# Kernel tuning notes

Hardware: AMD Instinct MI355X
Metric: run time of the kernel (lower is better)

Reference implementation:

```python
import jax, jax.numpy as jnp
import numpy as np

B, N, D, H = 4, 2048, 768, 12
HD = D // H  # head_dim = 64


def setup_inputs() -> dict:
    key = jax.random.key(0)
    k1, k2, k3 = jax.random.split(key, 3)
    z = jax.random.normal(k1, (B, N, D), dtype=jnp.float32)
    # per-head qkv Linear weights, torch Linear convention: y = x @ W.T + b
    Wqkv = jax.random.normal(k2, (H, 3 * HD, D), dtype=jnp.float32) * 0.02
    bqkv = jnp.zeros((H, 3 * HD), dtype=jnp.float32)
    Wmsa = jax.random.normal(k3, (D, D), dtype=jnp.float32) * 0.02
    bmsa = jnp.zeros((D,), dtype=jnp.float32)
    return {"z": z, "Wqkv": Wqkv, "bqkv": bqkv, "Wmsa": Wmsa, "bmsa": bmsa}


def reference(z, Wqkv, bqkv, Wmsa, bmsa):
    # All heads' qkv projections in one einsum: [B,N,D] x [H,3hd,D] -> [B,H,N,3hd]
    qkv = jnp.einsum("bnd,hed->bhne", z, Wqkv) + bqkv[None, :, None, :]
    q, k, v = jnp.split(qkv, 3, axis=-1)  # each [B,H,N,hd]
    scale = 1.0 / jnp.sqrt(jnp.asarray(HD, dtype=z.dtype))
    scores = jnp.einsum("bhqd,bhkd->bhqk", q, k) * scale  # [B,H,N,N]
    attn = jax.nn.softmax(scores, axis=-1)
    out = jnp.einsum("bhqk,bhkd->bhqd", attn, v)  # [B,H,N,hd]
    # concat heads (head order matches the torch per-head cat)
    out = out.transpose(0, 2, 1, 3).reshape(B, N, H * HD)  # [B,N,D]
    return out @ Wmsa.T + bmsa
```

## Files before the change

### kernel.cpp

```cpp
#include <hip/hip_runtime.h>

typedef unsigned short u16;
typedef unsigned int u32;
typedef __attribute__((ext_vector_type(8))) short bf16x8;
typedef __attribute__((ext_vector_type(4))) float f32x4;

#define B_ 4
#define H_ 12
#define N_ 2048
#define D_ 768
#define HD_ 64
#define NTOK (B_ * N_)
#define NE   (H_ * 3 * HD_)

#define BK 64
#define CPITCH 144

#define QSCALE 0.18033688011112042f

__device__ __forceinline__ u16 f2bf(float f) {
    u32 u = __float_as_uint(f);
    u += 0x7fffu + ((u >> 16) & 1u);
    return (u16)(u >> 16);
}

__device__ __forceinline__ f32x4 mfma16(bf16x8 a, bf16x8 b, f32x4 c) {
    return __builtin_amdgcn_mfma_f32_16x16x32_bf16(a, b, c, 0, 0, 0);
}

__device__ __forceinline__ void g2l16(const u16* g, u16* l) {
    __builtin_amdgcn_global_load_lds(
        (const __attribute__((address_space(1))) void*)g,
        (__attribute__((address_space(3))) void*)l, 16, 0, 0);
}

#define NZ4  (NTOK * D_ / 4)
#define NWQ4 (NE * D_ / 4)
#define NWM4 (D_ * D_ / 4)
__global__ __launch_bounds__(256) void cvt_all(const float* __restrict__ z,
                                               const float* __restrict__ Wq,
                                               const float* __restrict__ Wm,
                                               u16* __restrict__ Xbf,
                                               u16* __restrict__ Wqb,
                                               u16* __restrict__ Wmb) {
    int i = blockIdx.x * blockDim.x + threadIdx.x;
    const float* src;
    u16* dst;
    int j;
    if (i < NZ4) {
        src = z; dst = Xbf; j = i;
    } else if (i < NZ4 + NWQ4) {
        src = Wq; dst = Wqb; j = i - NZ4;
    } else if (i < NZ4 + NWQ4 + NWM4) {
        src = Wm; dst = Wmb; j = i - NZ4 - NWQ4;
    } else {
        return;
    }
    float4 v = ((const float4*)src)[j];
    u32 lo = (u32)f2bf(v.x) | ((u32)f2bf(v.y) << 16);
    u32 hi = (u32)f2bf(v.z) | ((u32)f2bf(v.w) << 16);
    ((uint2*)dst)[j] = make_uint2(lo, hi);
}

#define GEMM_CORE(Xp, Wp, TM, SMELEMS)                                         \
    __shared__ u16 smem[SMELEMS];                                              \
    u16* ldsA = smem;                                          \
    u16* ldsB = smem + 2 * (TM) * BK;                         \
    const int tid = threadIdx.x;                                               \
    const int wave = tid >> 6, lane = tid & 63;                                \
    const int lrow = lane & 15, quad = lane >> 4;                              \
    const int mbase = blockIdx.x * (TM);                                       \
    const int nbase = blockIdx.y * 128;                                        \
    const int srow = tid >> 3;                                      \
    const int schunk = tid & 7;                                                \
    const int sk = (schunk ^ (srow & 7)) << 3;   \
    const int sdst = srow * BK + schunk * 8;     \
    const u16* gA = Xp + (size_t)(mbase + srow) * D_ + sk;                     \
    const u16* gB = Wp + (size_t)(nbase + srow) * D_ + sk;                     \
    const int m_ofs = (wave >> 1) * ((TM) / 2);                                \
    const int n_ofs = (wave & 1) * 64;                                         \
    const int e_ = lrow & 7;                                                   \
    const int offA0 = (m_ofs + lrow) * BK + ((quad ^ e_) << 3);                \
    const int offB0 = (n_ofs + lrow) * BK + ((quad ^ e_) << 3);                \
    f32x4 acc[(TM) / 32][4] = {};                                              \
    _Pragma("unroll") for (int i = 0; i < (TM) / 32; i++)                      \
        g2l16(gA + (size_t)(32 * i) * D_, ldsA + sdst + i * 32 * BK);          \
    _Pragma("unroll") for (int i = 0; i < 4; i++)                              \
        g2l16(gB + (size_t)(32 * i) * D_, ldsB + sdst + i * 32 * BK);          \
    for (int it = 0; it < D_ / BK; it++) {                                     \
        const int cur = it & 1;                                                \
        const int abase = cur * (TM) * BK, bbase = cur * 128 * BK;             \
        __syncthreads();   \
        if (it + 1 < D_ / BK) {                                                \
            const int kt2 = (it + 1) * BK;                                     \
            const int nb = cur ^ 1;                                            \
            _Pragma("unroll") for (int i = 0; i < (TM) / 32; i++)              \
                g2l16(gA + (size_t)(32 * i) * D_ + kt2,                        \
                      ldsA + nb * (TM) * BK + sdst + i * 32 * BK);             \
            _Pragma("unroll") for (int i = 0; i < 4; i++)                      \
                g2l16(gB + (size_t)(32 * i) * D_ + kt2,                        \
                      ldsB + nb * 128 * BK + sdst + i * 32 * BK);              \
        }                                                                      \
        _Pragma("unroll") for (int ks = 0; ks < 2; ks++) {                     \
            const int oa = abase + (offA0 ^ (ks << 5));                        \
            const int ob = bbase + (offB0 ^ (ks << 5));                        \
            bf16x8 af[(TM) / 32], bfr[4];                                      \
            _Pragma("unroll") for (int c = 0; c < (TM) / 32; c++)              \
                af[c] = *(const bf16x8*)&ldsA[oa + c * 16 * BK];               \
            _Pragma("unroll") for (int c = 0; c < 4; c++)                      \
                bfr[c] = *(const bf16x8*)&ldsB[ob + c * 16 * BK];              \
            _Pragma("unroll") for (int i = 0; i < (TM) / 32; i++)              \
                _Pragma("unroll") for (int j = 0; j < 4; j++)                  \
                    acc[i][j] = mfma16(af[i], bfr[j], acc[i][j]);              \
        }                                                                      \
    }

__global__ __launch_bounds__(256) void gemm_qkv(const u16* __restrict__ X,
                                                const u16* __restrict__ W,
                                                const float* __restrict__ bqkv,
                                                u16* __restrict__ Qs,
                                                u16* __restrict__ Ks,
                                                u16* __restrict__ Vt) {
    GEMM_CORE(X, W, 64, 24576)
    __syncthreads();
    u16* ldsC = smem;
#pragma unroll
    for (int cn = 0; cn < 4; cn++) {
        const int E = nbase + n_ofs + cn * 16;
        const int h = E / 192;
        const int rr = E - h * 192;
        const int kind = rr >> 6;
        const float bias = bqkv[E + lrow];
        if (kind == 2) {
            const int d = (rr & 63) + lrow;
#pragma unroll
            for (int cm = 0; cm < 2; cm++) {
                const int t0 = mbase + m_ofs + cm * 16 + quad * 4;
                const int b_ = t0 >> 11, n0 = t0 & (N_ - 1);
                const size_t bh = (size_t)(b_ * H_ + h);
                uint2 pk;
                pk.x = (u32)f2bf(acc[cm][cn][0] + bias) |
                       ((u32)f2bf(acc[cm][cn][1] + bias) << 16);
                pk.y = (u32)f2bf(acc[cm][cn][2] + bias) |
                       ((u32)f2bf(acc[cm][cn][3] + bias) << 16);
                *(uint2*)&Vt[(bh * HD_ + d) * N_ + n0] = pk;
            }
        } else {
            const int fcol = n_ofs + cn * 16 + lrow;
            const float scale = (kind == 0) ? QSCALE : 1.0f;
#pragma unroll
            for (int cm = 0; cm < 2; cm++)
#pragma unroll
                for (int r = 0; r < 4; r++) {
                    const int tok = m_ofs + cm * 16 + quad * 4 + r;
                    ldsC[tok * CPITCH + fcol] =
                        f2bf((acc[cm][cn][r] + bias) * scale);
                }
        }
    }
    __syncthreads();
    {
        const int tok = tid >> 2, sub = tid & 3;
        const int fh = sub >> 1, jh = sub & 1;
        const int gf = nbase + fh * 64;
        const int kind2 = (gf >> 6) % 3;
        if (kind2 != 2) {
            const int h2 = gf / 192;
            const int t = mbase + tok;
            const int b2 = t >> 11, n2 = t & (N_ - 1);
            u16* dst = (kind2 == 0 ? Qs : Ks) +
                       ((size_t)(b2 * H_ + h2) * N_ + n2) * HD_;
            const u16* src = &ldsC[tok * CPITCH + fh * 64];
#pragma unroll
            for (int j = 0; j < 4; j++)
                *(uint4*)&dst[(jh * 4 + j) * 8] =
                    *(const uint4*)&src[(jh * 4 + j) * 8];
        }
    }
}

__global__ __launch_bounds__(256) void gemm_out(const u16* __restrict__ X2,
                                                const u16* __restrict__ W,
                                                const float* __restrict__ bmsa,
                                                float* __restrict__ out) {
    GEMM_CORE(X2, W, 64, 24576)
#pragma unroll
    for (int cn = 0; cn < 4; cn++) {
        const int col = nbase + n_ofs + cn * 16 + lrow;
        const float bias = bmsa[col];
#pragma unroll
        for (int cm = 0; cm < 2; cm++) {
#pragma unroll
            for (int r = 0; r < 4; r++) {
                const int t = mbase + m_ofs + cm * 16 + quad * 4 + r;
                out[(size_t)t * D_ + col] = acc[cm][cn][r] + bias;
            }
        }
    }
}

__global__ __launch_bounds__(256, 3) void flash_attn(const u16* __restrict__ Qs,
                                                     const u16* __restrict__ Ks,
                                                     const u16* __restrict__ Vt,
                                                     u16* __restrict__ X2) {
    __shared__ u16 ldsK[2][64 * HD_];
    __shared__ u16 ldsV[2][64 * HD_];
    __shared__ u16 ldsP[4][2][16][68];
    const int tid = threadIdx.x;
    const int wave = tid >> 6, lane = tid & 63;
    const int lrow = lane & 15, quad = lane >> 4;
    const int qbase = blockIdx.x * 128 + wave * 32;
    const int bh = blockIdx.y;
    const int b = bh / H_, h = bh - b * H_;

    const u16* Kb = Ks + (size_t)bh * N_ * HD_;
    const u16* Vb = Vt + (size_t)bh * HD_ * N_;

    const int srow = tid >> 3;
    const int schunk = tid & 7;
    const int skk = (schunk ^ (srow & 7)) << 3;
    const int sdst = srow * HD_ + schunk * 8;

    bf16x8 qa[2][2];
#pragma unroll
    for (int t = 0; t < 2; t++) {
        const u16* Qb = Qs + ((size_t)bh * N_ + qbase + t * 16 + lrow) * HD_ + quad * 8;
        qa[t][0] = *(const bf16x8*)(Qb);
        qa[t][1] = *(const bf16x8*)(Qb + 32);
    }

    const int fofs = (quad ^ (lrow & 7)) << 3;
    const short onebf = (short)0x3F80;
    const bf16x8 ones = {onebf, onebf, onebf, onebf, onebf, onebf, onebf, onebf};

    f32x4 Oacc[2][4] = {};
    f32x4 lacc[2] = {};

    {
        const u16* gK = Kb + (size_t)srow * HD_ + skk;
        g2l16(gK, &ldsK[0][sdst]);
        g2l16(gK + (size_t)32 * HD_, &ldsK[0][sdst + 32 * HD_]);
        const u16* gV = Vb + (size_t)srow * N_ + skk;
        g2l16(gV, &ldsV[0][sdst]);
        g2l16(gV + (size_t)32 * N_, &ldsV[0][sdst + 32 * HD_]);
    }

    for (int it = 0; it < N_ / 64; it++) {
        const int cur = it & 1;
        __syncthreads();
        if (it + 1 < N_ / 64) {
            const int kt2 = (it + 1) << 6;
            const u16* gK = Kb + (size_t)(kt2 + srow) * HD_ + skk;
            g2l16(gK, &ldsK[cur ^ 1][sdst]);
            g2l16(gK + (size_t)32 * HD_, &ldsK[cur ^ 1][sdst + 32 * HD_]);
            const u16* gV = Vb + (size_t)srow * N_ + kt2 + skk;
            g2l16(gV, &ldsV[cur ^ 1][sdst]);
            g2l16(gV + (size_t)32 * N_, &ldsV[cur ^ 1][sdst + 32 * HD_]);
        }
        bf16x8 kf[8];
#pragma unroll
        for (int c = 0; c < 4; c++) {
            const int o = (c * 16 + lrow) * HD_ + fofs;
            kf[2 * c]     = *(const bf16x8*)&ldsK[cur][o];
            kf[2 * c + 1] = *(const bf16x8*)&ldsK[cur][o ^ 32];
        }
        f32x4 s[2][4] = {};
#pragma unroll
        for (int t = 0; t < 2; t++)
#pragma unroll
            for (int c = 0; c < 4; c++) {
                s[t][c] = mfma16(kf[2 * c], qa[t][0], s[t][c]);
                s[t][c] = mfma16(kf[2 * c + 1], qa[t][1], s[t][c]);
            }
#pragma unroll
        for (int t = 0; t < 2; t++)
#pragma unroll
            for (int c = 0; c < 4; c++) {
                u32 b0 = __float_as_uint(__builtin_amdgcn_exp2f(s[t][c][0]));
                u32 b1 = __float_as_uint(__builtin_amdgcn_exp2f(s[t][c][1]));
                u32 b2 = __float_as_uint(__builtin_amdgcn_exp2f(s[t][c][2]));
                u32 b3 = __float_as_uint(__builtin_amdgcn_exp2f(s[t][c][3]));
                uint2 pk;
                pk.x = __builtin_amdgcn_perm(b1, b0, 0x07060302u);
                pk.y = __builtin_amdgcn_perm(b3, b2, 0x07060302u);
                *(uint2*)&ldsP[wave][t][lrow][c * 16 + quad * 4] = pk;
            }
        bf16x8 pa[2][2];
#pragma unroll
        for (int t = 0; t < 2; t++) {
            pa[t][0] = *(const bf16x8*)&ldsP[wave][t][lrow][quad * 8];
            pa[t][1] = *(const bf16x8*)&ldsP[wave][t][lrow][32 + quad * 8];
        }
#pragma unroll
        for (int t = 0; t < 2; t++) {
            lacc[t] = mfma16(pa[t][0], ones, lacc[t]);
            lacc[t] = mfma16(pa[t][1], ones, lacc[t]);
        }
#pragma unroll
        for (int c = 0; c < 4; c++) {
            const int o = (c * 16 + lrow) * HD_ + fofs;
            bf16x8 v0 = *(const bf16x8*)&ldsV[cur][o];
            bf16x8 v1 = *(const bf16x8*)&ldsV[cur][o ^ 32];
#pragma unroll
            for (int t = 0; t < 2; t++) {
                Oacc[t][c] = mfma16(pa[t][0], v0, Oacc[t][c]);
                Oacc[t][c] = mfma16(pa[t][1], v1, Oacc[t][c]);
            }
        }
    }
#pragma unroll
    for (int t = 0; t < 2; t++)
#pragma unroll
        for (int r = 0; r < 4; r++) {
            const float inv = 1.0f / lacc[t][r];
            const int qrow = qbase + t * 16 + quad * 4 + r;
#pragma unroll
            for (int c = 0; c < 4; c++) {
                X2[((size_t)b * N_ + qrow) * D_ + h * HD_ + c * 16 + lrow] =
                    f2bf(Oacc[t][c][r] * inv);
            }
        }
}

extern "C" void kernel_launch(void* const* d_in, const int* in_sizes, int n_in,
                              void* d_out, int out_size, void* d_ws, size_t ws_size,
                              hipStream_t stream) {
    const float* z    = (const float*)d_in[0];
    const float* Wqkv = (const float*)d_in[1];
    const float* bqkv = (const float*)d_in[2];
    const float* Wmsa = (const float*)d_in[3];
    const float* bmsa = (const float*)d_in[4];
    float* out = (float*)d_out;

    u16* Xbf = (u16*)d_ws;
    u16* Wqb = Xbf + (size_t)NTOK * D_;
    u16* Wmb = Wqb + (size_t)NE * D_;
    u16* Qs  = Wmb + (size_t)D_ * D_;
    u16* Ks  = Qs + (size_t)B_ * H_ * N_ * HD_;
    u16* Vt  = Ks + (size_t)B_ * H_ * N_ * HD_;
    u16* X2  = Vt + (size_t)B_ * H_ * N_ * HD_;

    const int ntot = NZ4 + NWQ4 + NWM4;
    cvt_all<<<(ntot + 255) / 256, 256, 0, stream>>>(z, Wqkv, Wmsa, Xbf, Wqb, Wmb);

    gemm_qkv<<<dim3(NTOK / 64, NE / 128), 256, 0, stream>>>(Xbf, Wqb, bqkv, Qs, Ks, Vt);
    flash_attn<<<dim3(N_ / 128, B_ * H_), 256, 0, stream>>>(Qs, Ks, Vt, X2);
    gemm_out<<<dim3(NTOK / 64, D_ / 128), 256, 0, stream>>>(X2, Wmb, bmsa, out);
}
```

Baseline: 204.9 us.

## Use two waves of 64 query rows each in flash attention blocks

```diff
diff --git a/kernel.cpp b/kernel.cpp
--- a/kernel.cpp
+++ b/kernel.cpp
@@ -199,17 +199,17 @@
     }
 }
 
-__global__ __launch_bounds__(256, 3) void flash_attn(const u16* __restrict__ Qs,
+__global__ __launch_bounds__(128, 2) void flash_attn(const u16* __restrict__ Qs,
                                                      const u16* __restrict__ Ks,
                                                      const u16* __restrict__ Vt,
                                                      u16* __restrict__ X2) {
     __shared__ u16 ldsK[2][64 * HD_];
     __shared__ u16 ldsV[2][64 * HD_];
-    __shared__ u16 ldsP[4][2][16][68];
+    __shared__ u16 ldsP[2][4][16][68];
     const int tid = threadIdx.x;
     const int wave = tid >> 6, lane = tid & 63;
     const int lrow = lane & 15, quad = lane >> 4;
-    const int qbase = blockIdx.x * 128 + wave * 32;
+    const int qbase = blockIdx.x * 128 + wave * 64;
     const int bh = blockIdx.y;
     const int b = bh / H_, h = bh - b * H_;
 
@@ -221,9 +221,9 @@
     const int skk = (schunk ^ (srow & 7)) << 3;
     const int sdst = srow * HD_ + schunk * 8;
 
-    bf16x8 qa[2][2];
-#pragma unroll
-    for (int t = 0; t < 2; t++) {
+    bf16x8 qa[4][2];
+#pragma unroll
+    for (int t = 0; t < 4; t++) {
         const u16* Qb = Qs + ((size_t)bh * N_ + qbase + t * 16 + lrow) * HD_ + quad * 8;
         qa[t][0] = *(const bf16x8*)(Qb);
         qa[t][1] = *(const bf16x8*)(Qb + 32);
@@ -233,16 +233,18 @@
     const short onebf = (short)0x3F80;
     const bf16x8 ones = {onebf, onebf, onebf, onebf, onebf, onebf, onebf, onebf};
 
-    f32x4 Oacc[2][4] = {};
-    f32x4 lacc[2] = {};
+    f32x4 Oacc[4][4] = {};
+    f32x4 lacc[4] = {};
 
     {
-        const u16* gK = Kb + (size_t)srow * HD_ + skk;
-        g2l16(gK, &ldsK[0][sdst]);
-        g2l16(gK + (size_t)32 * HD_, &ldsK[0][sdst + 32 * HD_]);
-        const u16* gV = Vb + (size_t)srow * N_ + skk;
-        g2l16(gV, &ldsV[0][sdst]);
-        g2l16(gV + (size_t)32 * N_, &ldsV[0][sdst + 32 * HD_]);
+#pragma unroll
+        for (int i = 0; i < 4; i++)
+            g2l16(Kb + (size_t)(16 * i + srow) * HD_ + skk,
+                  &ldsK[0][sdst + i * 16 * HD_]);
+#pragma unroll
+        for (int i = 0; i < 4; i++)
+            g2l16(Vb + (size_t)(16 * i + srow) * N_ + skk,
+                  &ldsV[0][sdst + i * 16 * HD_]);
     }
 
     for (int it = 0; it < N_ / 64; it++) {
@@ -250,12 +252,14 @@
         __syncthreads();
         if (it + 1 < N_ / 64) {
             const int kt2 = (it + 1) << 6;
-            const u16* gK = Kb + (size_t)(kt2 + srow) * HD_ + skk;
-            g2l16(gK, &ldsK[cur ^ 1][sdst]);
-            g2l16(gK + (size_t)32 * HD_, &ldsK[cur ^ 1][sdst + 32 * HD_]);
-            const u16* gV = Vb + (size_t)srow * N_ + kt2 + skk;
-            g2l16(gV, &ldsV[cur ^ 1][sdst]);
-            g2l16(gV + (size_t)32 * N_, &ldsV[cur ^ 1][sdst + 32 * HD_]);
+#pragma unroll
+            for (int i = 0; i < 4; i++)
+                g2l16(Kb + (size_t)(kt2 + 16 * i + srow) * HD_ + skk,
+                      &ldsK[cur ^ 1][sdst + i * 16 * HD_]);
+#pragma unroll
+            for (int i = 0; i < 4; i++)
+                g2l16(Vb + (size_t)(16 * i + srow) * N_ + kt2 + skk,
+                      &ldsV[cur ^ 1][sdst + i * 16 * HD_]);
         }
         bf16x8 kf[8];
 #pragma unroll
@@ -264,35 +268,34 @@
             kf[2 * c]     = *(const bf16x8*)&ldsK[cur][o];
             kf[2 * c + 1] = *(const bf16x8*)&ldsK[cur][o ^ 32];
         }
-        f32x4 s[2][4] = {};
-#pragma unroll
-        for (int t = 0; t < 2; t++)
+#pragma unroll
+        for (int t = 0; t < 4; t++) {
+            f32x4 st[4] = {};
 #pragma unroll
             for (int c = 0; c < 4; c++) {
-                s[t][c] = mfma16(kf[2 * c], qa[t][0], s[t][c]);
-                s[t][c] = mfma16(kf[2 * c + 1], qa[t][1], s[t][c]);
-            }
-#pragma unroll
-        for (int t = 0; t < 2; t++)
+                st[c] = mfma16(kf[2 * c], qa[t][0], st[c]);
+                st[c] = mfma16(kf[2 * c + 1], qa[t][1], st[c]);
+            }
 #pragma unroll
             for (int c = 0; c < 4; c++) {
-                u32 b0 = __float_as_uint(__builtin_amdgcn_exp2f(s[t][c][0]));
-                u32 b1 = __float_as_uint(__builtin_amdgcn_exp2f(s[t][c][1]));
-                u32 b2 = __float_as_uint(__builtin_amdgcn_exp2f(s[t][c][2]));
-                u32 b3 = __float_as_uint(__builtin_amdgcn_exp2f(s[t][c][3]));
+                u32 b0 = __float_as_uint(__builtin_amdgcn_exp2f(st[c][0]));
+                u32 b1 = __float_as_uint(__builtin_amdgcn_exp2f(st[c][1]));
+                u32 b2 = __float_as_uint(__builtin_amdgcn_exp2f(st[c][2]));
+                u32 b3 = __float_as_uint(__builtin_amdgcn_exp2f(st[c][3]));
                 uint2 pk;
                 pk.x = __builtin_amdgcn_perm(b1, b0, 0x07060302u);
                 pk.y = __builtin_amdgcn_perm(b3, b2, 0x07060302u);
                 *(uint2*)&ldsP[wave][t][lrow][c * 16 + quad * 4] = pk;
             }
-        bf16x8 pa[2][2];
-#pragma unroll
-        for (int t = 0; t < 2; t++) {
+        }
+        bf16x8 pa[4][2];
+#pragma unroll
+        for (int t = 0; t < 4; t++) {
             pa[t][0] = *(const bf16x8*)&ldsP[wave][t][lrow][quad * 8];
             pa[t][1] = *(const bf16x8*)&ldsP[wave][t][lrow][32 + quad * 8];
         }
 #pragma unroll
-        for (int t = 0; t < 2; t++) {
+        for (int t = 0; t < 4; t++) {
             lacc[t] = mfma16(pa[t][0], ones, lacc[t]);
             lacc[t] = mfma16(pa[t][1], ones, lacc[t]);
         }
@@ -302,14 +305,14 @@
             bf16x8 v0 = *(const bf16x8*)&ldsV[cur][o];
             bf16x8 v1 = *(const bf16x8*)&ldsV[cur][o ^ 32];
 #pragma unroll
-            for (int t = 0; t < 2; t++) {
+            for (int t = 0; t < 4; t++) {
                 Oacc[t][c] = mfma16(pa[t][0], v0, Oacc[t][c]);
                 Oacc[t][c] = mfma16(pa[t][1], v1, Oacc[t][c]);
             }
         }
     }
 #pragma unroll
-    for (int t = 0; t < 2; t++)
+    for (int t = 0; t < 4; t++)
 #pragma unroll
         for (int r = 0; r < 4; r++) {
             const float inv = 1.0f / lacc[t][r];
@@ -344,6 +347,6 @@
     cvt_all<<<(ntot + 255) / 256, 256, 0, stream>>>(z, Wqkv, Wmsa, Xbf, Wqb, Wmb);
 
     gemm_qkv<<<dim3(NTOK / 64, NE / 128), 256, 0, stream>>>(Xbf, Wqb, bqkv, Qs, Ks, Vt);
-    flash_attn<<<dim3(N_ / 128, B_ * H_), 256, 0, stream>>>(Qs, Ks, Vt, X2);
+    flash_attn<<<dim3(N_ / 128, B_ * H_), 128, 0, stream>>>(Qs, Ks, Vt, X2);
     gemm_out<<<dim3(NTOK / 64, D_ / 128), 256, 0, stream>>>(X2, Wmb, bmsa, out);
 }
```

After: 217.6 us. +6.2%, slower.
